# Optimization experiments

Measured on AMD Instinct MI355X. Metric: run time of the kernel, lower is better.

Reference implementation:

```python
import jax, jax.numpy as jnp
import numpy as np

B, T, D, H, HD = 2, 2048, 1024, 16, 64
EPS = 1.1920929e-07  # torch.finfo(float32).eps used by F.rms_norm default
VE_GATE_SCALE = 2.0
KEY_OFFSET = True


def rms_norm(x):
    return x * jax.lax.rsqrt(jnp.mean(x * x, axis=-1, keepdims=True) + EPS)


def apply_rotary(x, cos, sin):
    # x: [B,T,H,HD], cos/sin: [T, HD//2]
    c = cos[None, :, None, :]
    s = sin[None, :, None, :]
    x1, x2 = jnp.split(x, 2, axis=-1)
    return jnp.concatenate([x1 * c + x2 * s, -x1 * s + x2 * c], axis=-1)


def setup_inputs() -> dict:
    key = jax.random.key(0)
    ks = jax.random.split(key, 8)
    bound = (3.0 ** 0.5) * (D ** -0.5)
    x = jax.random.normal(ks[0], (B, T, D), dtype=jnp.float32)
    ve = jax.random.normal(ks[1], (B, T, H * HD), dtype=jnp.float32)
    sa_lambdas = jnp.ones((2,), dtype=jnp.float32)
    # realistic RoPE tables
    inv_freq = (10000.0 ** (-np.arange(HD // 2) / (HD // 2))).astype(np.float32)
    ang = np.arange(T, dtype=np.float32)[:, None] * inv_freq[None, :]
    cos = jnp.asarray(np.cos(ang))
    sin = jnp.asarray(np.sin(ang))
    # qkvo weight: uniform init everywhere (orig zeros o-proj; randomized for a non-trivial baseline)
    qkvo_w = jax.random.uniform(ks[2], (4 * D, D), dtype=jnp.float32, minval=-bound, maxval=bound)
    attn_gate_w = 0.02 * jax.random.normal(ks[3], (H, D), dtype=jnp.float32)
    ve_gate_w = 0.02 * jax.random.normal(ks[4], (H, D), dtype=jnp.float32)
    attn_scale = jnp.float32(0.12)
    docs = jnp.sort(jax.random.randint(ks[5], (T,), 0, 8).astype(jnp.int32))
    return {"x": x, "ve": ve, "sa_lambdas": sa_lambdas, "cos": cos, "sin": sin,
            "qkvo_w": qkvo_w, "attn_gate_w": attn_gate_w, "ve_gate_w": ve_gate_w,
            "attn_scale": attn_scale, "docs": docs}


def reference(x, ve, sa_lambdas, cos, sin, qkvo_w, attn_gate_w, ve_gate_w, attn_scale, docs):
    # QKV projection: rows [0:3D] of qkvo_w
    qkv = jnp.einsum('btd,ed->bte', x, sa_lambdas[0] * qkvo_w[:3 * D])
    qkv = qkv.reshape(B, T, 3 * H, HD)
    q, k, v = qkv[:, :, :H], qkv[:, :, H:2 * H], qkv[:, :, 2 * H:]
    q, k = rms_norm(q), rms_norm(k)
    q, k = apply_rotary(q, cos, sin), apply_rotary(k, cos, sin)
    if KEY_OFFSET:
        # shift two head-dim bands of k forward by one position
        k = k.at[:, 1:, :, HD // 4:HD // 2].set(k[:, :-1, :, HD // 4:HD // 2])
        k = k.at[:, 1:, :, 3 * HD // 4:].set(k[:, :-1, :, 3 * HD // 4:])
    # gated value embedding
    ve_gate = VE_GATE_SCALE * jax.nn.sigmoid(jnp.einsum('btd,hd->bth', x, ve_gate_w))
    v = v + ve_gate[..., None] * ve.reshape(B, T, H, HD)
    # causal + document masked attention (score_mod semantics)
    idx = jnp.arange(T)
    mask = (idx[:, None] >= idx[None, :]) & (docs[:, None] == docs[None, :])  # [T,T]
    scores = jnp.einsum('bqhd,bkhd->bhqk', q, k) * attn_scale
    scores = jnp.where(mask[None, None], scores, -jnp.inf)
    p = jax.nn.softmax(scores, axis=-1)
    y = jnp.einsum('bhqk,bkhd->bqhd', p, v)
    # attention output gate
    attn_gate = jax.nn.sigmoid(jnp.einsum('btd,hd->bth', x, attn_gate_w))
    y = y * attn_gate[..., None]
    # output projection: rows [3D:4D]
    y = y.reshape(B, T, H * HD)
    out = jnp.einsum('btd,ed->bte', y, sa_lambdas[1] * qkvo_w[3 * D:])
    return out
```

## Files before the change

### kernel.cpp

```cpp
#include <hip/hip_runtime.h>
#include <math.h>

#define B_ 2
#define T_ 2048
#define D_ 1024
#define H_ 16
#define HD_ 64
#define EPS_ 1.1920929e-07f
#define VE_SCALE_ 2.0f

#define NX4_ (B_ * T_ * D_ / 4)
#define NS4_ (3 * D_ * D_ / 4)
#define NQ4_ (4 * D_ * D_ / 4)
#define NG4_ (H_ * D_ / 4)

typedef __bf16 bf16_t;
typedef __bf16 bf16x4 __attribute__((ext_vector_type(4)));
typedef __bf16 bf16x8 __attribute__((ext_vector_type(8)));
typedef float f32x4 __attribute__((ext_vector_type(4)));

__device__ const f32x4 F4ZERO = {0.f, 0.f, 0.f, 0.f};

typedef __attribute__((address_space(1))) const void gvoid_t;
typedef __attribute__((address_space(3))) void lvoid_t;

__device__ __forceinline__ void gl_lds16(const bf16_t* g, bf16_t* l) {
  __builtin_amdgcn_global_load_lds((gvoid_t*)g, (lvoid_t*)l, 16, 0, 0);
}

__global__ __launch_bounds__(256) void cast_all(
    const float* __restrict__ x, const float* __restrict__ qkvo,
    const float* __restrict__ agw, const float* __restrict__ vgw,
    bf16_t* __restrict__ x_bf, bf16_t* __restrict__ wq,
    bf16_t* __restrict__ wo, bf16_t* __restrict__ wg)
{
  const int i = blockIdx.x * 256 + threadIdx.x;
  const float4* src;
  bf16x4* dst;
  if (i < NX4_) {
    src = (const float4*)x + i;
    dst = (bf16x4*)x_bf + i;
  } else if (i < NX4_ + NS4_) {
    const int j = i - NX4_;
    src = (const float4*)qkvo + j;
    dst = (bf16x4*)wq + j;
  } else if (i < NX4_ + NQ4_) {
    const int j = i - NX4_;
    src = (const float4*)qkvo + j;
    dst = (bf16x4*)wo + (j - NS4_);
  } else if (i < NX4_ + NQ4_ + NG4_) {
    const int j = i - NX4_ - NQ4_;
    src = (const float4*)agw + j;
    dst = (bf16x4*)wg + j;
  } else {
    const int j = i - NX4_ - NQ4_ - NG4_;
    src = (const float4*)vgw + j;
    dst = (bf16x4*)wg + NG4_ + j;
  }
  const float4 v = *src;
  bf16x4 o = {(bf16_t)v.x, (bf16_t)v.y, (bf16_t)v.z, (bf16_t)v.w};
  *dst = o;
}

__global__ __launch_bounds__(256) void gates_kernel(
    const bf16_t* __restrict__ x_bf, const bf16_t* __restrict__ wg,
    float* __restrict__ attn_gate, float* __restrict__ ve_gate2)
{
  const int bt = blockIdx.x;
  const int tid = threadIdx.x;
  __shared__ float xs[D_];
  {
    const bf16x4 xv = ((const bf16x4*)(x_bf + (size_t)bt * D_))[tid];
    xs[tid * 4 + 0] = (float)xv[0];
    xs[tid * 4 + 1] = (float)xv[1];
    xs[tid * 4 + 2] = (float)xv[2];
    xs[tid * 4 + 3] = (float)xv[3];
  }
  __syncthreads();
  const int g = tid >> 3, cg = tid & 7;
  const bf16x8* wrow = (const bf16x8*)(wg + (size_t)g * D_);
  float sum = 0.f;
#pragma unroll
  for (int j = 0; j < 16; ++j) {
    const bf16x8 w8 = wrow[cg + 8 * j];
    const float* xp = &xs[(cg + 8 * j) * 8];
#pragma unroll
    for (int e = 0; e < 8; ++e) sum = fmaf((float)w8[e], xp[e], sum);
  }
  sum += __shfl_xor(sum, 1);
  sum += __shfl_xor(sum, 2);
  sum += __shfl_xor(sum, 4);
  if (cg == 0) {
    const float sg = 1.f / (1.f + __expf(-sum));
    if (g < 16) attn_gate[bt * H_ + g] = sg;
    else        ve_gate2[bt * H_ + (g - 16)] = VE_SCALE_ * sg;
  }
}

__global__ __launch_bounds__(512) void gemm_qkv(
    const bf16_t* __restrict__ A, const bf16_t* __restrict__ W,
    const float* __restrict__ ve, const float* __restrict__ cosb,
    const float* __restrict__ sinb, const float* __restrict__ ve_gate2,
    bf16_t* __restrict__ q_bf, bf16_t* __restrict__ k_bf,
    bf16_t* __restrict__ v_bf, int K,
    const float* __restrict__ lam)
{
  const float scale = lam[0];
  __shared__ bf16_t As[2][128][32];
  __shared__ bf16_t Bs[2][128][32];
  const int tid = threadIdx.x;
  const int lane = tid & 63, w = tid >> 6;
  const int lr = lane & 15, lg = lane >> 4;
  const int wr = w >> 1, wc = w & 1;

  const int nwg = gridDim.x * gridDim.y;
  int bid = blockIdx.y * gridDim.x + blockIdx.x;
  bid = (bid & 7) * (nwg >> 3) + (bid >> 3);
  const int row0 = (bid / gridDim.x) * 128;
  const int col0 = (bid % gridDim.x) * 128;

  const int srow = w * 16 + (lane >> 2);
  const int scol = (lane & 3) * 8;
  const bf16_t* Ag = A + (size_t)(row0 + srow) * K + scol;
  const bf16_t* Wg = W + (size_t)(col0 + srow) * K + scol;

  f32x4 acc[2][4];
#pragma unroll
  for (int i = 0; i < 2; ++i)
#pragma unroll
    for (int j = 0; j < 4; ++j) acc[i][j] = F4ZERO;

#define STAGE_(bi, kk)                            \
  do {                                            \
    gl_lds16(Ag + (kk), &As[bi][w * 16][0]);      \
    gl_lds16(Wg + (kk), &Bs[bi][w * 16][0]);      \
  } while (0)

#define COMPUTE_(bi)                                                     \
  do {                                                                   \
    bf16x8 af[2], bfr[4];                                                \
    _Pragma("unroll")                                                    \
    for (int fm = 0; fm < 2; ++fm)                                       \
      af[fm] = *(const bf16x8*)&As[bi][wr * 32 + fm * 16 + lr][lg * 8];  \
    _Pragma("unroll")                                                    \
    for (int fn = 0; fn < 4; ++fn)                                       \
      bfr[fn] = *(const bf16x8*)&Bs[bi][wc * 64 + fn * 16 + lr][lg * 8]; \
    _Pragma("unroll")                                                    \
    for (int fm = 0; fm < 2; ++fm)                                       \
      _Pragma("unroll")                                                  \
      for (int fn = 0; fn < 4; ++fn)                                     \
        acc[fm][fn] = __builtin_amdgcn_mfma_f32_16x16x32_bf16(           \
            af[fm], bfr[fn], acc[fm][fn], 0, 0, 0);                      \
  } while (0)

  STAGE_(0, 0);
  __syncthreads();
  for (int k0 = 0; k0 + 64 <= K; k0 += 64) {
    STAGE_(1, k0 + 32);
    COMPUTE_(0);
    __syncthreads();
    if (k0 + 64 < K) STAGE_(0, k0 + 64);
    COMPUTE_(1);
    __syncthreads();
  }
#undef STAGE_
#undef COMPUTE_

  const int sec = col0 >> 10;
  const int h = ((col0 & 1023) >> 6) + wc;
#pragma unroll
  for (int fm = 0; fm < 2; ++fm) {
#pragma unroll
    for (int r = 0; r < 4; ++r) {
      const int row = row0 + wr * 32 + fm * 16 + lg * 4 + r;
      const int b = row >> 11, t = row & (T_ - 1);
      float v0 = acc[fm][0][r] * scale;
      float v1 = acc[fm][1][r] * scale;
      float v2 = acc[fm][2][r] * scale;
      float v3 = acc[fm][3][r] * scale;
      const size_t obase = ((size_t)(b * H_ + h) * T_ + t) * HD_;
      if (sec < 2) {
        float ssq = v0 * v0 + v1 * v1 + v2 * v2 + v3 * v3;
        ssq += __shfl_xor(ssq, 1);
        ssq += __shfl_xor(ssq, 2);
        ssq += __shfl_xor(ssq, 4);
        ssq += __shfl_xor(ssq, 8);
        const float rn = rsqrtf(ssq * (1.f / 64.f) + EPS_);
        v0 *= rn; v1 *= rn; v2 *= rn; v3 *= rn;
        const float c0 = cosb[t * 32 + lr], s0 = sinb[t * 32 + lr];
        const float c1 = cosb[t * 32 + 16 + lr], s1 = sinb[t * 32 + 16 + lr];
        const float o0 = fmaf(v0, c0, v2 * s0);
        const float o2 = fmaf(v2, c0, -v0 * s0);
        const float o1 = fmaf(v1, c1, v3 * s1);
        const float o3 = fmaf(v3, c1, -v1 * s1);
        bf16_t* dst = (sec == 0 ? q_bf : k_bf);
        dst[obase + 0 + lr]  = (bf16_t)o0;
        dst[obase + 16 + lr] = (bf16_t)o1;
        dst[obase + 32 + lr] = (bf16_t)o2;
        dst[obase + 48 + lr] = (bf16_t)o3;
      } else {
        const float g = ve_gate2[row * H_ + h];
        const float* vp = ve + (size_t)row * D_ + h * HD_;
        v0 = fmaf(g, vp[0 + lr], v0);
        v1 = fmaf(g, vp[16 + lr], v1);
        v2 = fmaf(g, vp[32 + lr], v2);
        v3 = fmaf(g, vp[48 + lr], v3);
        v_bf[obase + 0 + lr]  = (bf16_t)v0;
        v_bf[obase + 16 + lr] = (bf16_t)v1;
        v_bf[obase + 32 + lr] = (bf16_t)v2;
        v_bf[obase + 48 + lr] = (bf16_t)v3;
      }
    }
  }
}

__global__ __launch_bounds__(256) void gemm_bf16(
    const bf16_t* __restrict__ A, const bf16_t* __restrict__ W,
    float* __restrict__ Cout, int M, int N, int K,
    const float* __restrict__ lam, int li)
{
  const float scale = lam[li];
  __shared__ bf16_t As[2][64][32];
  __shared__ bf16_t Bs[2][128][32];
  const int tid = threadIdx.x;
  const int lane = tid & 63, w = tid >> 6;
  const int lr = lane & 15, lg = lane >> 4;
  const int wr = w >> 1, wc = w & 1;

  const int nwg = gridDim.x * gridDim.y;
  int bid = blockIdx.y * gridDim.x + blockIdx.x;
  bid = (bid & 7) * (nwg >> 3) + (bid >> 3);
  const int row0 = (bid / gridDim.x) * 64;
  const int col0 = (bid % gridDim.x) * 128;

  const int srow = lane >> 2;
  const int scol = (lane & 3) * 8;
  const bf16_t* Ag  = A + (size_t)(row0 + w * 16 + srow) * K + scol;
  const bf16_t* Wg0 = W + (size_t)(col0 + w * 16 + srow) * K + scol;
  const bf16_t* Wg1 = Wg0 + (size_t)64 * K;

  f32x4 acc[2][4];
#pragma unroll
  for (int i = 0; i < 2; ++i)
#pragma unroll
    for (int j = 0; j < 4; ++j) acc[i][j] = F4ZERO;

#define STAGE_(bi, kk)                                \
  do {                                                \
    gl_lds16(Ag + (kk), &As[bi][w * 16][0]);          \
    gl_lds16(Wg0 + (kk), &Bs[bi][w * 16][0]);         \
    gl_lds16(Wg1 + (kk), &Bs[bi][64 + w * 16][0]);    \
  } while (0)

#define COMPUTE_(bi)                                                     \
  do {                                                                   \
    bf16x8 af[2], bfr[4];                                                \
    _Pragma("unroll")                                                    \
    for (int fm = 0; fm < 2; ++fm)                                       \
      af[fm] = *(const bf16x8*)&As[bi][wr * 32 + fm * 16 + lr][lg * 8];  \
    _Pragma("unroll")                                                    \
    for (int fn = 0; fn < 4; ++fn)                                       \
      bfr[fn] = *(const bf16x8*)&Bs[bi][wc * 64 + fn * 16 + lr][lg * 8]; \
    _Pragma("unroll")                                                    \
    for (int fm = 0; fm < 2; ++fm)                                       \
      _Pragma("unroll")                                                  \
      for (int fn = 0; fn < 4; ++fn)                                     \
        acc[fm][fn] = __builtin_amdgcn_mfma_f32_16x16x32_bf16(           \
            af[fm], bfr[fn], acc[fm][fn], 0, 0, 0);                      \
  } while (0)

  STAGE_(0, 0);
  __syncthreads();
  for (int k0 = 0; k0 + 64 <= K; k0 += 64) {
    STAGE_(1, k0 + 32);
    COMPUTE_(0);
    __syncthreads();
    if (k0 + 64 < K) STAGE_(0, k0 + 64);
    COMPUTE_(1);
    __syncthreads();
  }
#undef STAGE_
#undef COMPUTE_

#pragma unroll
  for (int fm = 0; fm < 2; ++fm)
#pragma unroll
    for (int fn = 0; fn < 4; ++fn)
#pragma unroll
      for (int r = 0; r < 4; ++r) {
        const int row = row0 + wr * 32 + fm * 16 + lg * 4 + r;
        const int col = col0 + wc * 64 + fn * 16 + lr;
        Cout[(size_t)row * N + col] = acc[fm][fn][r] * scale;
      }
}

__global__ __launch_bounds__(256) void attn_mfma(
    const bf16_t* __restrict__ q_buf, const bf16_t* __restrict__ k_tmp,
    const bf16_t* __restrict__ v_buf, const float* __restrict__ attn_gate,
    const int* __restrict__ docs, const float* __restrict__ scale_ptr,
    bf16_t* __restrict__ y_buf)
{
  const int qt = blockIdx.x, bh = blockIdx.y;
  const int b = bh >> 4, h = bh & 15;
  const int tid = threadIdx.x;
  const int w = tid >> 6, lane = tid & 63;
  const int lr = lane & 15, lg = lane >> 4;
  const float scale = scale_ptr[0];
  __shared__ bf16_t Ks[64][72];
  __shared__ bf16_t Vt[64][72];
  __shared__ bf16_t Ps[64][72];
  __shared__ int dk[64];

  const int dlo = docs[qt * 64];
  const unsigned long long bal =
      __ballot((lane <= qt) && (docs[lane * 64 + 63] >= dlo));
  const int ktlo = __ffsll(bal) - 1;

  const bf16_t* qp = q_buf + ((size_t)bh * T_ + qt * 64 + w * 16 + lr) * HD_;
  const bf16x8 aq0 = *(const bf16x8*)(qp + lg * 8);
  const bf16x8 aq1 = *(const bf16x8*)(qp + 32 + lg * 8);
  int qpos_r[4], docq_r[4];
#pragma unroll
  for (int r = 0; r < 4; ++r) {
    qpos_r[r] = qt * 64 + w * 16 + lg * 4 + r;
    docq_r[r] = docs[qpos_r[r]];
  }
  f32x4 acc[4];
#pragma unroll
  for (int fn = 0; fn < 4; ++fn) acc[fn] = F4ZERO;
  float m[4] = {-1e30f, -1e30f, -1e30f, -1e30f};
  float l[4] = {0.f, 0.f, 0.f, 0.f};

  bf16x8 rk[2], rv[2];
#define LOADREGS_(ktt)                                                        \
  do {                                                                        \
    _Pragma("unroll")                                                         \
    for (int i = 0; i < 2; ++i) {                                             \
      const int idx = i * 256 + tid;                                          \
      const int krow = idx >> 3;                                              \
      const int c8 = (idx & 7) << 3;                                          \
      const int gk = (ktt) * 64 + krow;                                       \
      const int gks = (((c8 & 16) != 0) && gk > 0) ? gk - 1 : gk;             \
      rk[i] = *(const bf16x8*)(k_tmp + ((size_t)bh * T_ + gks) * HD_ + c8);   \
      const int kpos = idx & 63;                                              \
      const int d0 = (idx >> 6) << 3;                                         \
      rv[i] = *(const bf16x8*)(v_buf +                                        \
               ((size_t)bh * T_ + (ktt) * 64 + kpos) * HD_ + d0);             \
    }                                                                         \
  } while (0)

  LOADREGS_(ktlo);

#pragma unroll 1
  for (int kt = ktlo; kt <= qt; ++kt) {
    __syncthreads();
#pragma unroll
    for (int i = 0; i < 2; ++i) {
      const int idx = i * 256 + tid;
      const int krow = idx >> 3;
      const int c8 = (idx & 7) << 3;
      *(bf16x8*)&Ks[krow][c8] = rk[i];
      const int kpos = idx & 63;
      const int d0 = (idx >> 6) << 3;
#pragma unroll
      for (int j = 0; j < 8; ++j) Vt[d0 + j][kpos] = rv[i][j];
    }
    if (tid < 64) dk[tid] = docs[kt * 64 + tid];
    __syncthreads();
    if (kt < qt) LOADREGS_(kt + 1);

    f32x4 s[4];
#pragma unroll
    for (int fn = 0; fn < 4; ++fn) {
      const bf16x8 bk0 = *(const bf16x8*)&Ks[fn * 16 + lr][lg * 8];
      const bf16x8 bk1 = *(const bf16x8*)&Ks[fn * 16 + lr][32 + lg * 8];
      f32x4 z = F4ZERO;
      z = __builtin_amdgcn_mfma_f32_16x16x32_bf16(aq0, bk0, z, 0, 0, 0);
      s[fn] = __builtin_amdgcn_mfma_f32_16x16x32_bf16(aq1, bk1, z, 0, 0, 0);
    }
    const bool strict = (kt < qt);
#pragma unroll
    for (int fn = 0; fn < 4; ++fn) {
      const int kd = dk[fn * 16 + lr];
      const int kp = kt * 64 + fn * 16 + lr;
#pragma unroll
      for (int r = 0; r < 4; ++r) {
        const bool valid = (kd == docq_r[r]) && (strict || kp <= qpos_r[r]);
        s[fn][r] = valid ? s[fn][r] * scale : -3.0e38f;
      }
    }
#pragma unroll
    for (int r = 0; r < 4; ++r) {
      float cm = fmaxf(fmaxf(s[0][r], s[1][r]), fmaxf(s[2][r], s[3][r]));
      cm = fmaxf(cm, __shfl_xor(cm, 1));
      cm = fmaxf(cm, __shfl_xor(cm, 2));
      cm = fmaxf(cm, __shfl_xor(cm, 4));
      cm = fmaxf(cm, __shfl_xor(cm, 8));
      const float mn = fmaxf(m[r], cm);
      const float sc = __expf(m[r] - mn);
      m[r] = mn;
      const float p0 = __expf(s[0][r] - mn);
      const float p1 = __expf(s[1][r] - mn);
      const float p2 = __expf(s[2][r] - mn);
      const float p3 = __expf(s[3][r] - mn);
      float ps = (p0 + p1) + (p2 + p3);
      ps += __shfl_xor(ps, 1);
      ps += __shfl_xor(ps, 2);
      ps += __shfl_xor(ps, 4);
      ps += __shfl_xor(ps, 8);
      l[r] = l[r] * sc + ps;
      acc[0][r] *= sc; acc[1][r] *= sc; acc[2][r] *= sc; acc[3][r] *= sc;
      const int prow = w * 16 + lg * 4 + r;
      Ps[prow][0 + lr]  = (bf16_t)p0;
      Ps[prow][16 + lr] = (bf16_t)p1;
      Ps[prow][32 + lr] = (bf16_t)p2;
      Ps[prow][48 + lr] = (bf16_t)p3;
    }
    const bf16x8 ap0 = *(const bf16x8*)&Ps[w * 16 + lr][lg * 8];
    const bf16x8 ap1 = *(const bf16x8*)&Ps[w * 16 + lr][32 + lg * 8];
#pragma unroll
    for (int fn = 0; fn < 4; ++fn) {
      const bf16x8 bv0 = *(const bf16x8*)&Vt[fn * 16 + lr][lg * 8];
      const bf16x8 bv1 = *(const bf16x8*)&Vt[fn * 16 + lr][32 + lg * 8];
      acc[fn] = __builtin_amdgcn_mfma_f32_16x16x32_bf16(ap0, bv0, acc[fn], 0, 0, 0);
      acc[fn] = __builtin_amdgcn_mfma_f32_16x16x32_bf16(ap1, bv1, acc[fn], 0, 0, 0);
    }
  }
#undef LOADREGS_
#pragma unroll
  for (int r = 0; r < 4; ++r) {
    const float inv = attn_gate[(size_t)(b * T_ + qpos_r[r]) * H_ + h] / l[r];
#pragma unroll
    for (int fn = 0; fn < 4; ++fn)
      y_buf[(size_t)(b * T_ + qpos_r[r]) * D_ + h * HD_ + fn * 16 + lr] =
          (bf16_t)(acc[fn][r] * inv);
  }
}

extern "C" void kernel_launch(void* const* d_in, const int* in_sizes, int n_in,
                              void* d_out, int out_size, void* d_ws, size_t ws_size,
                              hipStream_t stream) {
  const float* x    = (const float*)d_in[0];
  const float* ve   = (const float*)d_in[1];
  const float* lam  = (const float*)d_in[2];
  const float* cosb = (const float*)d_in[3];
  const float* sinb = (const float*)d_in[4];
  const float* qkvo = (const float*)d_in[5];
  const float* agw  = (const float*)d_in[6];
  const float* vgw  = (const float*)d_in[7];
  const float* ascl = (const float*)d_in[8];
  const int*   docs = (const int*)d_in[9];
  float* out = (float*)d_out;

  const size_t BT = (size_t)B_ * T_;
  float* cur = (float*)d_ws;
  bf16_t* x_bf = (bf16_t*)cur;        cur += BT * D_ / 2;
  bf16_t* wq_bf = (bf16_t*)cur;       cur += (size_t)3 * D_ * D_ / 2;
  bf16_t* wo_bf = (bf16_t*)cur;       cur += (size_t)D_ * D_ / 2;
  bf16_t* wg_bf = (bf16_t*)cur;       cur += (size_t)2 * H_ * D_ / 2;
  bf16_t* q_bf = (bf16_t*)cur;        cur += BT * D_ / 2;
  bf16_t* k_bf = (bf16_t*)cur;        cur += BT * D_ / 2;
  bf16_t* v_bf = (bf16_t*)cur;        cur += BT * D_ / 2;
  bf16_t* y_bf = (bf16_t*)cur;        cur += BT * D_ / 2;
  float* attn_gate = cur;             cur += BT * H_;
  float* ve_gate2 = cur;              cur += BT * H_;

  cast_all<<<(NX4_ + NQ4_ + 2 * NG4_) / 256, 256, 0, stream>>>(
      x, qkvo, agw, vgw, x_bf, wq_bf, wo_bf, wg_bf);

  gates_kernel<<<(int)BT, 256, 0, stream>>>(x_bf, wg_bf, attn_gate, ve_gate2);

  gemm_qkv<<<dim3(3 * D_ / 128, BT / 128), 512, 0, stream>>>(
      x_bf, wq_bf, ve, cosb, sinb, ve_gate2, q_bf, k_bf, v_bf, D_, lam);

  attn_mfma<<<dim3(T_ / 64, B_ * H_), 256, 0, stream>>>(
      q_bf, k_bf, v_bf, attn_gate, docs, ascl, y_bf);

  gemm_bf16<<<dim3(D_ / 128, BT / 64), 256, 0, stream>>>(
      y_bf, wo_bf, out, (int)BT, D_, D_, lam, 1);
}
```

Before: 115.9 us.

## Restructure QKV GEMM mainloop with 64-wide K tiles, XOR-swizzled LDS and split staging

The QKV projection GEMM now stages 64-wide K slices instead of 32, and stores them in LDS with an XOR swizzle on the 16-byte chunk index to avoid bank conflicts on the fragment reads. The main loop is split into two half-phases with explicit vmcnt/lgkmcnt waits, raw s_barriers and setprio around MFMA bursts. Next-tile B loads are issued during the first half and next-tile A loads during the second, so global-to-LDS traffic overlaps with matrix math. LDS use doubles and the hand-written wait counts are fragile, so the correctness of the synchronisation depends on the exact counts.

```diff
diff --git a/kernel.cpp b/kernel.cpp
--- a/kernel.cpp
+++ b/kernel.cpp
@@ -106,8 +106,8 @@
     const float* __restrict__ lam)
 {
   const float scale = lam[0];
-  __shared__ bf16_t As[2][128][32];
-  __shared__ bf16_t Bs[2][128][32];
+  __shared__ bf16_t As[2][128][64];
+  __shared__ bf16_t Bs[2][128][64];
   const int tid = threadIdx.x;
   const int lane = tid & 63, w = tid >> 6;
   const int lr = lane & 15, lg = lane >> 4;
@@ -119,10 +119,24 @@
   const int row0 = (bid / gridDim.x) * 128;
   const int col0 = (bid % gridDim.x) * 128;
 
-  const int srow = w * 16 + (lane >> 2);
-  const int scol = (lane & 3) * 8;
-  const bf16_t* Ag = A + (size_t)(row0 + srow) * K + scol;
-  const bf16_t* Wg = W + (size_t)(col0 + srow) * K + scol;
+  const int srow8 = lane >> 3;
+  const int sg8 = (lane & 7) ^ srow8;
+  const bf16_t* Agl = A + (size_t)(row0 + srow8) * K + sg8 * 8;
+  const bf16_t* Wgl = W + (size_t)(col0 + srow8) * K + sg8 * 8;
+
+  const int arow0 = (w >> 1) * 32 + (w & 1) * 8;
+  const int brow0 = w * 16;
+
+#define STA_(buf, j, kk)                                          \
+  gl_lds16(Agl + (size_t)(arow0 + (j) * 16) * K + (kk),           \
+           &As[buf][arow0 + (j) * 16][0])
+#define STB_(buf, hf, kk)                                         \
+  gl_lds16(Wgl + (size_t)(brow0 + (hf) * 8) * K + (kk),           \
+           &Bs[buf][brow0 + (hf) * 8][0])
+#define LDA_(buf, fm, kh) \
+  (*(const bf16x8*)&As[buf][wr * 32 + (fm) * 16 + lr][((((kh) * 4) + lg) ^ (lr & 7)) * 8])
+#define LDB_(buf, fn, kh) \
+  (*(const bf16x8*)&Bs[buf][wc * 64 + (fn) * 16 + lr][((((kh) * 4) + lg) ^ (lr & 7)) * 8])
 
   f32x4 acc[2][4];
 #pragma unroll
@@ -130,41 +144,63 @@
 #pragma unroll
     for (int j = 0; j < 4; ++j) acc[i][j] = F4ZERO;
 
-#define STAGE_(bi, kk)                            \
-  do {                                            \
-    gl_lds16(Ag + (kk), &As[bi][w * 16][0]);      \
-    gl_lds16(Wg + (kk), &Bs[bi][w * 16][0]);      \
-  } while (0)
-
-#define COMPUTE_(bi)                                                     \
-  do {                                                                   \
-    bf16x8 af[2], bfr[4];                                                \
-    _Pragma("unroll")                                                    \
-    for (int fm = 0; fm < 2; ++fm)                                       \
-      af[fm] = *(const bf16x8*)&As[bi][wr * 32 + fm * 16 + lr][lg * 8];  \
-    _Pragma("unroll")                                                    \
-    for (int fn = 0; fn < 4; ++fn)                                       \
-      bfr[fn] = *(const bf16x8*)&Bs[bi][wc * 64 + fn * 16 + lr][lg * 8]; \
-    _Pragma("unroll")                                                    \
-    for (int fm = 0; fm < 2; ++fm)                                       \
-      _Pragma("unroll")                                                  \
-      for (int fn = 0; fn < 4; ++fn)                                     \
-        acc[fm][fn] = __builtin_amdgcn_mfma_f32_16x16x32_bf16(           \
-            af[fm], bfr[fn], acc[fm][fn], 0, 0, 0);                      \
-  } while (0)
-
-  STAGE_(0, 0);
-  __syncthreads();
-  for (int k0 = 0; k0 + 64 <= K; k0 += 64) {
-    STAGE_(1, k0 + 32);
-    COMPUTE_(0);
-    __syncthreads();
-    if (k0 + 64 < K) STAGE_(0, k0 + 64);
-    COMPUTE_(1);
-    __syncthreads();
-  }
-#undef STAGE_
-#undef COMPUTE_
+  STB_(0, 0, 0); STB_(0, 1, 0); STA_(0, 0, 0); STA_(0, 1, 0);
+
+  const int nt = K >> 6;
+  bf16x8 bfr[4][2];
+  for (int kt = 0; kt < nt; ++kt) {
+    const int cur = kt & 1, nxt = cur ^ 1;
+    const int kn = (kt + 1) << 6;
+    const bool more = (kt + 1) < nt;
+    asm volatile("s_waitcnt vmcnt(1)" ::: "memory");
+    __builtin_amdgcn_s_barrier();
+    {
+      bf16x8 a00, a01;
+#pragma unroll
+      for (int fn = 0; fn < 4; ++fn) {
+        bfr[fn][0] = LDB_(cur, fn, 0);
+        bfr[fn][1] = LDB_(cur, fn, 1);
+      }
+      a00 = LDA_(cur, 0, 0); a01 = LDA_(cur, 0, 1);
+      if (more) { STB_(nxt, 0, kn); STB_(nxt, 1, kn); }
+      asm volatile("s_waitcnt lgkmcnt(0)" ::: "memory");
+      __builtin_amdgcn_sched_barrier(0);
+      __builtin_amdgcn_s_setprio(1);
+#pragma unroll
+      for (int fn = 0; fn < 4; ++fn) {
+        acc[0][fn] = __builtin_amdgcn_mfma_f32_16x16x32_bf16(
+            a00, bfr[fn][0], acc[0][fn], 0, 0, 0);
+        acc[0][fn] = __builtin_amdgcn_mfma_f32_16x16x32_bf16(
+            a01, bfr[fn][1], acc[0][fn], 0, 0, 0);
+      }
+      __builtin_amdgcn_s_setprio(0);
+    }
+    __builtin_amdgcn_s_barrier();
+    if (more) asm volatile("s_waitcnt vmcnt(2)" ::: "memory");
+    else      asm volatile("s_waitcnt vmcnt(0)" ::: "memory");
+    __builtin_amdgcn_s_barrier();
+    {
+      bf16x8 a10, a11;
+      a10 = LDA_(cur, 1, 0); a11 = LDA_(cur, 1, 1);
+      if (more) { STA_(nxt, 0, kn); STA_(nxt, 1, kn); }
+      asm volatile("s_waitcnt lgkmcnt(0)" ::: "memory");
+      __builtin_amdgcn_sched_barrier(0);
+      __builtin_amdgcn_s_setprio(1);
+#pragma unroll
+      for (int fn = 0; fn < 4; ++fn) {
+        acc[1][fn] = __builtin_amdgcn_mfma_f32_16x16x32_bf16(
+            a10, bfr[fn][0], acc[1][fn], 0, 0, 0);
+        acc[1][fn] = __builtin_amdgcn_mfma_f32_16x16x32_bf16(
+            a11, bfr[fn][1], acc[1][fn], 0, 0, 0);
+      }
+      __builtin_amdgcn_s_setprio(0);
+    }
+    __builtin_amdgcn_s_barrier();
+  }
+#undef STA_
+#undef STB_
+#undef LDA_
+#undef LDB_
 
   const int sec = col0 >> 10;
   const int h = ((col0 & 1023) >> 6) + wc;
```

New measurement: 120.3 us. +3.8%, slower.
